# Kernel optimization log

Hardware: AMD Instinct MI355X
Metric: run time of the kernel (lower is better)

## Reference

```python
import jax, jax.numpy as jnp
import numpy as np

# Static hyperparameters (match init_kwargs)
PAD = 4          # one_side_pad_length
KL = 9           # kernel_size (= 2*PAD + 1 so L_out == output_size with stride 1)
STRIDE = 1
NLC = 8          # num_sparse_LC
OUT = 4096       # output_size


def _repeat_lengths():
    padded = OUT + 2 * PAD                      # 4104
    rough = padded // NLC                       # 513
    lens = []
    total = 0
    for i in range(NLC):
        if i == NLC - 1:
            cover = OUT - total
        else:
            cover = rough - 2 * PAD
        lens.append(cover)
        total += cover
    return lens                                  # [505]*7 + [561]


def setup_inputs() -> dict:
    key = jax.random.key(0)
    k1, k2, k3 = jax.random.split(key, 3)
    x = jax.random.normal(k1, (8, 2, 4, 64, 4096), dtype=jnp.float32)
    # weight: (dim_d, dim_k, out, in, num_sparse_LC, 1, kernel_size)
    weight = jax.random.normal(k2, (2, 4, 64, 64, 8, 1, 9), dtype=jnp.float32) * 0.05
    # conv_bias_param: (dim_d, dim_k, out, num_sparse_LC, 1)
    conv_bias_param = jax.random.normal(k3, (2, 4, 64, 8, 1), dtype=jnp.float32) * 0.02
    return {"x": x, "weight": weight, "conv_bias_param": conv_bias_param}


def reference(x, weight, conv_bias_param):
    # x: (b, d, k, in, L)
    x_pad = jnp.pad(x, ((0, 0), (0, 0), (0, 0), (0, 0), (PAD, PAD)))
    # unfold(-1, KL, 1): x_unf[..., l, f] = x_pad[..., l + f]; shape (b,d,k,in,OUT,KL)
    x_unf = jnp.stack([x_pad[..., f:f + OUT] for f in range(KL)], axis=-1)
    lens = _repeat_lengths()
    outs = []
    start = 0
    for i in range(NLC):  # small fixed loop over segments (avoids repeated-weight materialization)
        ln = lens[i]
        w = weight[:, :, :, :, i, 0, :]                 # (d, k, o, in, kl)
        xs = x_unf[:, :, :, :, start:start + ln, :]     # (b, d, k, in, ln, kl)
        o = jnp.einsum('dkoif,bdkilf->bdkol', w, xs)    # (b, d, k, o, ln)
        o = o + conv_bias_param[None, :, :, :, i, :]    # bias broadcasts over b and l
        outs.append(o)
        start += ln
    return jnp.concatenate(outs, axis=-1)               # (b, d, k, o, OUT)
```

## Files before the change

kernel.cpp:

```cpp
#include <hip/hip_runtime.h>

typedef __attribute__((ext_vector_type(8))) short bf16x8;
typedef __attribute__((ext_vector_type(4))) float f32x4;

#define WT2_BYTES (8ull * 8 * 9 * 8192)

static __device__ __forceinline__ ushort f2bf(float f) {
    union { float f; unsigned u; } v; v.f = f;
    unsigned r = v.u + 0x7FFF + ((v.u >> 16) & 1);
    return (ushort)(r >> 16);
}
static __device__ __forceinline__ unsigned cvtpk(float a, float b) {
    unsigned r;
    asm("v_cvt_pk_bf16_f32 %0, %1, %2" : "=v"(r) : "v"(a), "v"(b));
    return r;
}

__global__ __launch_bounds__(256) void wprep3_kernel(const float* __restrict__ w,
                                                     ushort* __restrict__ wt) {
    __shared__ float raw[4608];
    __shared__ ushort row[72 * 64];
    int bid = blockIdx.x;
    int dk = bid >> 6, o = bid & 63;
    const float* src = w + (size_t)bid * 4608;
    int t = threadIdx.x;
    #pragma unroll
    for (int j = 0; j < 18; ++j) raw[t + 256 * j] = src[t + 256 * j];
    __syncthreads();
    int osw = o & 7;
    #pragma unroll
    for (int p = 0; p < 18; ++p) {
        int idx = t + 256 * p;
        int cf = idx >> 6, i = idx & 63;
        int c = cf / 9, f = cf - c * 9;
        row[cf * 64 + ((i >> 3) ^ osw) * 8 + (i & 7)] = f2bf(raw[i * 72 + c * 9 + f]);
    }
    __syncthreads();
    char* wb = (char*)wt + (size_t)dk * 8 * 9 * 8192 + o * 128;
    #pragma unroll
    for (int q = 0; q < 3; ++q) {
        int idx = q * 256 + t;
        if (idx < 576) {
            int cf = idx >> 3, cc = idx & 7;
            *(uint4*)(wb + (size_t)cf * 8192 + cc * 16) = *(const uint4*)&row[cf * 64 + cc * 8];
        }
    }
}

__global__ __launch_bounds__(512, 4) void conv12_kernel(
    const float* __restrict__ x, const ushort* __restrict__ wt,
    const float* __restrict__ bias, float* __restrict__ out)
{
    __shared__ __align__(16) ushort XL[264 * 64];

    int bid = blockIdx.x;
    int b = bid / 136, rem = bid - b * 136;
    int dk = rem / 17, tile = rem - dk * 17;
    int c, lt;
    if (tile < 14) { c = tile >> 1; lt = tile & 1; } else { c = 7; lt = tile - 14; }
    int Sc = 505 * c, lb = lt << 8;
    int V = ((c == 7) ? 561 : 505) - lb; if (V > 256) V = 256;
    int bdk = b * 8 + dk;
    int R0 = Sc + lb;

    int t = threadIdx.x, lane = t & 63, wv = t >> 6;
    int ln16 = lane & 15, g = lane >> 4;
    int wr = wv >> 1, wc = wv & 1;
    int Lw = wr << 6, Ow = wc << 5;

    int lq = t & 63, ig = t >> 6;
    const float* xb = x + (size_t)bdk * 64 * 4096;
    float4 v[8];
    bool edge = (R0 < 4) || (R0 > 3836);
    if (!edge) {
        const float* xp = xb + (size_t)ig * 8 * 4096 + (R0 - 4 + lq * 4);
        #pragma unroll
        for (int j = 0; j < 8; ++j)
            v[j] = *(const float4*)(xp + (size_t)j * 4096);
    } else {
        #pragma unroll
        for (int j = 0; j < 8; ++j) {
            float* pv = (float*)&v[j];
            #pragma unroll
            for (int k = 0; k < 4; ++k) {
                int xr = R0 - 4 + lq * 4 + k;
                bool ok = (xr >= 0) && (xr < 4096);
                int xc = ok ? xr : 0;
                pv[k] = ok ? xb[(size_t)(ig * 8 + j) * 4096 + xc] : 0.0f;
            }
        }
    }
    float hv[8]; int rh = 0, igh = 0;
    if (t < 64) {
        rh = 256 + (t >> 3);
        igh = t & 7;
        int xr = R0 - 4 + rh;
        bool okh = xr < 4096;
        int xc = okh ? xr : 0;
        const float* xh = xb + (size_t)igh * 8 * 4096 + xc;
        #pragma unroll
        for (int j = 0; j < 8; ++j) hv[j] = okh ? xh[(size_t)j * 4096] : 0.0f;
    }

    const char* wsl = (const char*)wt + (size_t)(dk * 8 + c) * 9 * 8192;
    int wo[2][2];
    #pragma unroll
    for (int s = 0; s < 2; ++s)
        #pragma unroll
        for (int nf = 0; nf < 2; ++nf)
            wo[s][nf] = (Ow + nf * 16 + ln16) * 128 + (((s * 4 + g) ^ (ln16 & 7)) * 16);

    bf16x8 w0[2][2], w1[2][2];
    auto loadW = [&](bf16x8 (&d)[2][2], int f) {
        const char* bp = wsl + (size_t)f * 8192;
        #pragma unroll
        for (int s = 0; s < 2; ++s)
            #pragma unroll
            for (int nf = 0; nf < 2; ++nf)
                d[s][nf] = *(const bf16x8*)(bp + wo[s][nf]);
    };
    loadW(w0, 0);

    #pragma unroll
    for (int k = 0; k < 4; ++k) {
        int r = lq * 4 + k;
        uint4 A;
        A.x = cvtpk(((const float*)&v[0])[k], ((const float*)&v[1])[k]);
        A.y = cvtpk(((const float*)&v[2])[k], ((const float*)&v[3])[k]);
        A.z = cvtpk(((const float*)&v[4])[k], ((const float*)&v[5])[k]);
        A.w = cvtpk(((const float*)&v[6])[k], ((const float*)&v[7])[k]);
        *(uint4*)((char*)XL + r * 128 + ((ig ^ (r & 7)) * 16)) = A;
    }
    if (t < 64) {
        uint4 A;
        A.x = cvtpk(hv[0], hv[1]); A.y = cvtpk(hv[2], hv[3]);
        A.z = cvtpk(hv[4], hv[5]); A.w = cvtpk(hv[6], hv[7]);
        *(uint4*)((char*)XL + rh * 128 + ((igh ^ (rh & 7)) * 16)) = A;
    }
    loadW(w1, 1);

    asm volatile("s_waitcnt lgkmcnt(0)" ::: "memory");
    __syncthreads();

    f32x4 acc[4][2];
    #pragma unroll
    for (int a0 = 0; a0 < 4; ++a0)
        #pragma unroll
        for (int a1 = 0; a1 < 2; ++a1) acc[a0][a1] = (f32x4){0.f, 0.f, 0.f, 0.f};

    auto tap = [&](int f, bf16x8 (&wf)[2][2]) {
        int rbase = Lw + ln16 + f;
        int swz = rbase & 7;
        #pragma unroll
        for (int s = 0; s < 2; ++s) {
            int cof = ((s * 4 + g) ^ swz) * 16;
            bf16x8 av[4];
            #pragma unroll
            for (int mf = 0; mf < 4; ++mf)
                av[mf] = *(const bf16x8*)((const char*)XL + (rbase + mf * 16) * 128 + cof);
            __builtin_amdgcn_s_setprio(1);
            #pragma unroll
            for (int mf = 0; mf < 4; ++mf)
                #pragma unroll
                for (int nf = 0; nf < 2; ++nf)
                    acc[mf][nf] = __builtin_amdgcn_mfma_f32_16x16x32_bf16(av[mf], wf[s][nf], acc[mf][nf], 0, 0, 0);
            __builtin_amdgcn_s_setprio(0);
        }
    };

    tap(0, w0); loadW(w0, 2);
    tap(1, w1); loadW(w1, 3);
    tap(2, w0); loadW(w0, 4);
    tap(3, w1); loadW(w1, 5);
    tap(4, w0); loadW(w0, 6);
    tap(5, w1); loadW(w1, 7);
    tap(6, w0); loadW(w0, 8);
    tap(7, w1);
    tap(8, w0);

    float* ob = out + ((size_t)(bdk * 64)) * 4096 + Sc + lb;
    #pragma unroll
    for (int nf = 0; nf < 2; ++nf) {
        int o = Ow + nf * 16 + ln16;
        float bvs = bias[(dk * 64 + o) * 8 + c];
        #pragma unroll
        for (int mf = 0; mf < 4; ++mf) {
            int l = Lw + mf * 16 + g * 4;
            f32x4 vv = acc[mf][nf];
            vv[0] += bvs; vv[1] += bvs; vv[2] += bvs; vv[3] += bvs;
            if (l + 4 <= V) {
                *(f32x4*)(ob + (size_t)o * 4096 + l) = vv;
            } else if (l < V) {
                #pragma unroll
                for (int r = 0; r < 4; ++r)
                    if (l + r < V) ob[(size_t)o * 4096 + l + r] = vv[r];
            }
        }
    }
}

extern "C" void kernel_launch(void* const* d_in, const int* in_sizes, int n_in,
                              void* d_out, int out_size, void* d_ws, size_t ws_size,
                              hipStream_t stream) {
    const float* x    = (const float*)d_in[0];
    const float* wgt  = (const float*)d_in[1];
    const float* bias = (const float*)d_in[2];
    float* out        = (float*)d_out;
    ushort* wt2       = (ushort*)d_ws;

    hipLaunchKernelGGL(wprep3_kernel, dim3(512), dim3(256), 0, stream, wgt, wt2);
    hipLaunchKernelGGL(conv12_kernel, dim3(1088), dim3(512), 0, stream, x, wt2, bias, out);
}
```

Baseline: 49.34 us.

## Process two tiles per block with double-buffered LDS to overlap loads

```diff
diff --git a/kernel.cpp b/kernel.cpp
--- a/kernel.cpp
+++ b/kernel.cpp
@@ -47,62 +47,29 @@
     }
 }
 
-__global__ __launch_bounds__(512, 4) void conv12_kernel(
+__global__ __launch_bounds__(512, 4) void conv13_kernel(
     const float* __restrict__ x, const ushort* __restrict__ wt,
     const float* __restrict__ bias, float* __restrict__ out)
 {
-    __shared__ __align__(16) ushort XL[264 * 64];
-
-    int bid = blockIdx.x;
-    int b = bid / 136, rem = bid - b * 136;
-    int dk = rem / 17, tile = rem - dk * 17;
-    int c, lt;
-    if (tile < 14) { c = tile >> 1; lt = tile & 1; } else { c = 7; lt = tile - 14; }
-    int Sc = 505 * c, lb = lt << 8;
-    int V = ((c == 7) ? 561 : 505) - lb; if (V > 256) V = 256;
-    int bdk = b * 8 + dk;
-    int R0 = Sc + lb;
+    __shared__ __align__(16) ushort XL[2][264 * 64];
 
     int t = threadIdx.x, lane = t & 63, wv = t >> 6;
     int ln16 = lane & 15, g = lane >> 4;
     int wr = wv >> 1, wc = wv & 1;
     int Lw = wr << 6, Ow = wc << 5;
-
     int lq = t & 63, ig = t >> 6;
-    const float* xb = x + (size_t)bdk * 64 * 4096;
-    float4 v[8];
-    bool edge = (R0 < 4) || (R0 > 3836);
-    if (!edge) {
-        const float* xp = xb + (size_t)ig * 8 * 4096 + (R0 - 4 + lq * 4);
-        #pragma unroll
-        for (int j = 0; j < 8; ++j)
-            v[j] = *(const float4*)(xp + (size_t)j * 4096);
-    } else {
-        #pragma unroll
-        for (int j = 0; j < 8; ++j) {
-            float* pv = (float*)&v[j];
-            #pragma unroll
-            for (int k = 0; k < 4; ++k) {
-                int xr = R0 - 4 + lq * 4 + k;
-                bool ok = (xr >= 0) && (xr < 4096);
-                int xc = ok ? xr : 0;
-                pv[k] = ok ? xb[(size_t)(ig * 8 + j) * 4096 + xc] : 0.0f;
-            }
-        }
-    }
-    float hv[8]; int rh = 0, igh = 0;
-    if (t < 64) {
-        rh = 256 + (t >> 3);
-        igh = t & 7;
-        int xr = R0 - 4 + rh;
-        bool okh = xr < 4096;
-        int xc = okh ? xr : 0;
-        const float* xh = xb + (size_t)igh * 8 * 4096 + xc;
-        #pragma unroll
-        for (int j = 0; j < 8; ++j) hv[j] = okh ? xh[(size_t)j * 4096] : 0.0f;
-    }
-
-    const char* wsl = (const char*)wt + (size_t)(dk * 8 + c) * 9 * 8192;
+
+    auto dec = [&](int tid, int& bdk, int& dk, int& c, int& V, int& R0) {
+        int b = tid / 136, rem = tid - b * 136;
+        dk = rem / 17; int tile = rem - dk * 17;
+        int lt;
+        if (tile < 14) { c = tile >> 1; lt = tile & 1; } else { c = 7; lt = tile - 14; }
+        int lb = lt << 8;
+        V = ((c == 7) ? 561 : 505) - lb; if (V > 256) V = 256;
+        R0 = 505 * c + lb;
+        bdk = b * 8 + dk;
+    };
+
     int wo[2][2];
     #pragma unroll
     for (int s = 0; s < 2; ++s)
@@ -110,6 +77,7 @@
         for (int nf = 0; nf < 2; ++nf)
             wo[s][nf] = (Ow + nf * 16 + ln16) * 128 + (((s * 4 + g) ^ (ln16 & 7)) * 16);
 
+    const char* wsl = nullptr;
     bf16x8 w0[2][2], w1[2][2];
     auto loadW = [&](bf16x8 (&d)[2][2], int f) {
         const char* bp = wsl + (size_t)f * 8192;
@@ -119,36 +87,63 @@
             for (int nf = 0; nf < 2; ++nf)
                 d[s][nf] = *(const bf16x8*)(bp + wo[s][nf]);
     };
-    loadW(w0, 0);
-
-    #pragma unroll
-    for (int k = 0; k < 4; ++k) {
-        int r = lq * 4 + k;
-        uint4 A;
-        A.x = cvtpk(((const float*)&v[0])[k], ((const float*)&v[1])[k]);
-        A.y = cvtpk(((const float*)&v[2])[k], ((const float*)&v[3])[k]);
-        A.z = cvtpk(((const float*)&v[4])[k], ((const float*)&v[5])[k]);
-        A.w = cvtpk(((const float*)&v[6])[k], ((const float*)&v[7])[k]);
-        *(uint4*)((char*)XL + r * 128 + ((ig ^ (r & 7)) * 16)) = A;
-    }
-    if (t < 64) {
-        uint4 A;
-        A.x = cvtpk(hv[0], hv[1]); A.y = cvtpk(hv[2], hv[3]);
-        A.z = cvtpk(hv[4], hv[5]); A.w = cvtpk(hv[6], hv[7]);
-        *(uint4*)((char*)XL + rh * 128 + ((igh ^ (rh & 7)) * 16)) = A;
-    }
-    loadW(w1, 1);
-
-    asm volatile("s_waitcnt lgkmcnt(0)" ::: "memory");
-    __syncthreads();
+
+    float4 vA[4], vB[4]; float hv[8];
+    auto issueHalf = [&](int bdkX, int R0X, int h, float4 (&v)[4]) {
+        const float* xb = x + (size_t)bdkX * 64 * 4096;
+        bool edge = (R0X < 4) || (R0X > 3836);
+        if (!edge) {
+            const float* xp = xb + (size_t)(ig * 8 + h * 4) * 4096 + (R0X - 4 + lq * 4);
+            #pragma unroll
+            for (int j = 0; j < 4; ++j)
+                v[j] = *(const float4*)(xp + (size_t)j * 4096);
+        } else {
+            #pragma unroll
+            for (int j = 0; j < 4; ++j) {
+                float* pv = (float*)&v[j];
+                #pragma unroll
+                for (int k = 0; k < 4; ++k) {
+                    int xr = R0X - 4 + lq * 4 + k;
+                    bool ok = (xr >= 0) && (xr < 4096);
+                    int xc = ok ? xr : 0;
+                    pv[k] = ok ? xb[(size_t)(ig * 8 + h * 4 + j) * 4096 + xc] : 0.0f;
+                }
+            }
+        }
+    };
+    auto issueHalo = [&](int bdkX, int R0X) {
+        if (t < 64) {
+            int rh = 256 + (t >> 3), igh = t & 7;
+            int xr = R0X - 4 + rh;
+            bool okh = xr < 4096;
+            int xc = okh ? xr : 0;
+            const float* xh = x + (size_t)bdkX * 64 * 4096 + (size_t)igh * 8 * 4096 + xc;
+            #pragma unroll
+            for (int j = 0; j < 8; ++j) hv[j] = okh ? xh[(size_t)j * 4096] : 0.0f;
+        }
+    };
+    auto writeTile = [&](ushort* dst) {
+        #pragma unroll
+        for (int k = 0; k < 4; ++k) {
+            int r = lq * 4 + k;
+            uint4 A;
+            A.x = cvtpk(((const float*)&vA[0])[k], ((const float*)&vA[1])[k]);
+            A.y = cvtpk(((const float*)&vA[2])[k], ((const float*)&vA[3])[k]);
+            A.z = cvtpk(((const float*)&vB[0])[k], ((const float*)&vB[1])[k]);
+            A.w = cvtpk(((const float*)&vB[2])[k], ((const float*)&vB[3])[k]);
+            *(uint4*)((char*)dst + r * 128 + ((ig ^ (r & 7)) * 16)) = A;
+        }
+        if (t < 64) {
+            int rh = 256 + (t >> 3), igh = t & 7;
+            uint4 A;
+            A.x = cvtpk(hv[0], hv[1]); A.y = cvtpk(hv[2], hv[3]);
+            A.z = cvtpk(hv[4], hv[5]); A.w = cvtpk(hv[6], hv[7]);
+            *(uint4*)((char*)dst + rh * 128 + ((igh ^ (rh & 7)) * 16)) = A;
+        }
+    };
 
     f32x4 acc[4][2];
-    #pragma unroll
-    for (int a0 = 0; a0 < 4; ++a0)
-        #pragma unroll
-        for (int a1 = 0; a1 < 2; ++a1) acc[a0][a1] = (f32x4){0.f, 0.f, 0.f, 0.f};
-
-    auto tap = [&](int f, bf16x8 (&wf)[2][2]) {
+    auto tap = [&](const char* xbuf, int f, bf16x8 (&wf)[2][2]) {
         int rbase = Lw + ln16 + f;
         int swz = rbase & 7;
         #pragma unroll
@@ -157,7 +152,7 @@
             bf16x8 av[4];
             #pragma unroll
             for (int mf = 0; mf < 4; ++mf)
-                av[mf] = *(const bf16x8*)((const char*)XL + (rbase + mf * 16) * 128 + cof);
+                av[mf] = *(const bf16x8*)(xbuf + (rbase + mf * 16) * 128 + cof);
             __builtin_amdgcn_s_setprio(1);
             #pragma unroll
             for (int mf = 0; mf < 4; ++mf)
@@ -167,36 +162,82 @@
             __builtin_amdgcn_s_setprio(0);
         }
     };
-
-    tap(0, w0); loadW(w0, 2);
-    tap(1, w1); loadW(w1, 3);
-    tap(2, w0); loadW(w0, 4);
-    tap(3, w1); loadW(w1, 5);
-    tap(4, w0); loadW(w0, 6);
-    tap(5, w1); loadW(w1, 7);
-    tap(6, w0); loadW(w0, 8);
-    tap(7, w1);
-    tap(8, w0);
-
-    float* ob = out + ((size_t)(bdk * 64)) * 4096 + Sc + lb;
-    #pragma unroll
-    for (int nf = 0; nf < 2; ++nf) {
-        int o = Ow + nf * 16 + ln16;
-        float bvs = bias[(dk * 64 + o) * 8 + c];
-        #pragma unroll
-        for (int mf = 0; mf < 4; ++mf) {
-            int l = Lw + mf * 16 + g * 4;
-            f32x4 vv = acc[mf][nf];
-            vv[0] += bvs; vv[1] += bvs; vv[2] += bvs; vv[3] += bvs;
-            if (l + 4 <= V) {
-                *(f32x4*)(ob + (size_t)o * 4096 + l) = vv;
-            } else if (l < V) {
-                #pragma unroll
-                for (int r = 0; r < 4; ++r)
-                    if (l + r < V) ob[(size_t)o * 4096 + l + r] = vv[r];
+    auto epilogue = [&](int bdk, int dk, int c, int V, int R0) {
+        float* ob = out + ((size_t)(bdk * 64)) * 4096 + R0;
+        #pragma unroll
+        for (int nf = 0; nf < 2; ++nf) {
+            int o = Ow + nf * 16 + ln16;
+            float bvs = bias[(dk * 64 + o) * 8 + c];
+            #pragma unroll
+            for (int mf = 0; mf < 4; ++mf) {
+                int l = Lw + mf * 16 + g * 4;
+                f32x4 vv = acc[mf][nf];
+                vv[0] += bvs; vv[1] += bvs; vv[2] += bvs; vv[3] += bvs;
+                if (l + 4 <= V) {
+                    *(f32x4*)(ob + (size_t)o * 4096 + l) = vv;
+                } else if (l < V) {
+                    #pragma unroll
+                    for (int r = 0; r < 4; ++r)
+                        if (l + r < V) ob[(size_t)o * 4096 + l + r] = vv[r];
+                }
             }
         }
-    }
+    };
+
+    int t0 = 2 * blockIdx.x, t1 = t0 + 1;
+    int bdk0, dk0, c0, V0, R00, bdk1, dk1, c1, V1, R01;
+    dec(t0, bdk0, dk0, c0, V0, R00);
+    dec(t1, bdk1, dk1, c1, V1, R01);
+
+    issueHalf(bdk0, R00, 0, vA);
+    issueHalf(bdk0, R00, 1, vB);
+    issueHalo(bdk0, R00);
+    writeTile(XL[0]);
+    __syncthreads();
+
+    wsl = (const char*)wt + (size_t)(dk0 * 8 + c0) * 9 * 8192;
+    loadW(w0, 0); loadW(w1, 1);
+    #pragma unroll
+    for (int a0 = 0; a0 < 4; ++a0)
+        #pragma unroll
+        for (int a1 = 0; a1 < 2; ++a1) acc[a0][a1] = (f32x4){0.f, 0.f, 0.f, 0.f};
+
+    issueHalf(bdk1, R01, 0, vA);
+    __builtin_amdgcn_sched_barrier(0);
+    const char* xc = (const char*)XL[0];
+    tap(xc, 0, w0); loadW(w0, 2);
+    tap(xc, 1, w1); loadW(w1, 3);
+    tap(xc, 2, w0); loadW(w0, 4);
+    tap(xc, 3, w1); loadW(w1, 5);
+    issueHalf(bdk1, R01, 1, vB);
+    issueHalo(bdk1, R01);
+    __builtin_amdgcn_sched_barrier(0);
+    tap(xc, 4, w0); loadW(w0, 6);
+    tap(xc, 5, w1); loadW(w1, 7);
+    tap(xc, 6, w0); loadW(w0, 8);
+    tap(xc, 7, w1);
+    tap(xc, 8, w0);
+    epilogue(bdk0, dk0, c0, V0, R00);
+    writeTile(XL[1]);
+    __syncthreads();
+
+    wsl = (const char*)wt + (size_t)(dk1 * 8 + c1) * 9 * 8192;
+    loadW(w0, 0); loadW(w1, 1);
+    #pragma unroll
+    for (int a0 = 0; a0 < 4; ++a0)
+        #pragma unroll
+        for (int a1 = 0; a1 < 2; ++a1) acc[a0][a1] = (f32x4){0.f, 0.f, 0.f, 0.f};
+    xc = (const char*)XL[1];
+    tap(xc, 0, w0); loadW(w0, 2);
+    tap(xc, 1, w1); loadW(w1, 3);
+    tap(xc, 2, w0); loadW(w0, 4);
+    tap(xc, 3, w1); loadW(w1, 5);
+    tap(xc, 4, w0); loadW(w0, 6);
+    tap(xc, 5, w1); loadW(w1, 7);
+    tap(xc, 6, w0); loadW(w0, 8);
+    tap(xc, 7, w1);
+    tap(xc, 8, w0);
+    epilogue(bdk1, dk1, c1, V1, R01);
 }
 
 extern "C" void kernel_launch(void* const* d_in, const int* in_sizes, int n_in,
@@ -209,5 +250,5 @@
     ushort* wt2       = (ushort*)d_ws;
 
     hipLaunchKernelGGL(wprep3_kernel, dim3(512), dim3(256), 0, stream, wgt, wt2);
-    hipLaunchKernelGGL(conv12_kernel, dim3(1088), dim3(512), 0, stream, x, wt2, bias, out);
-}
+    hipLaunchKernelGGL(conv13_kernel, dim3(544), dim3(512), 0, stream, x, wt2, bias, out);
+}
```

Measured after the change: 75.43 us. 52.9% more time.

## Pre-transpose x to padded bf16 in prep kernel; drop LDS staging in conv

Applied to the files above, without the earlier changes.

```diff
diff --git a/kernel.cpp b/kernel.cpp
--- a/kernel.cpp
+++ b/kernel.cpp
@@ -3,6 +3,8 @@
 typedef __attribute__((ext_vector_type(8))) short bf16x8;
 typedef __attribute__((ext_vector_type(4))) float f32x4;
 
+#define XT_ROWS 4104
+#define XT_STRIDE ((size_t)XT_ROWS * 128)
 #define WT2_BYTES (8ull * 8 * 9 * 8192)
 
 static __device__ __forceinline__ ushort f2bf(float f) {
@@ -16,43 +18,86 @@
     return r;
 }
 
-__global__ __launch_bounds__(256) void wprep3_kernel(const float* __restrict__ w,
-                                                     ushort* __restrict__ wt) {
+__global__ __launch_bounds__(256) void prep_kernel(const float* __restrict__ w,
+                                                   const float* __restrict__ x,
+                                                   ushort* __restrict__ wt,
+                                                   ushort* __restrict__ xT) {
     __shared__ float raw[4608];
     __shared__ ushort row[72 * 64];
+    __shared__ ushort XB[128 * 72];
     int bid = blockIdx.x;
-    int dk = bid >> 6, o = bid & 63;
-    const float* src = w + (size_t)bid * 4608;
     int t = threadIdx.x;
-    #pragma unroll
-    for (int j = 0; j < 18; ++j) raw[t + 256 * j] = src[t + 256 * j];
-    __syncthreads();
-    int osw = o & 7;
-    #pragma unroll
-    for (int p = 0; p < 18; ++p) {
-        int idx = t + 256 * p;
-        int cf = idx >> 6, i = idx & 63;
-        int c = cf / 9, f = cf - c * 9;
-        row[cf * 64 + ((i >> 3) ^ osw) * 8 + (i & 7)] = f2bf(raw[i * 72 + c * 9 + f]);
+    if (bid < 512) {
+        int dk = bid >> 6, o = bid & 63;
+        const float* src = w + (size_t)bid * 4608;
+        #pragma unroll
+        for (int j = 0; j < 18; ++j) raw[t + 256 * j] = src[t + 256 * j];
+        __syncthreads();
+        int osw = o & 7;
+        #pragma unroll
+        for (int p = 0; p < 18; ++p) {
+            int idx = t + 256 * p;
+            int cf = idx >> 6, i = idx & 63;
+            int c = cf / 9, f = cf - c * 9;
+            row[cf * 64 + ((i >> 3) ^ osw) * 8 + (i & 7)] = f2bf(raw[i * 72 + c * 9 + f]);
+        }
+        __syncthreads();
+        char* wb = (char*)wt + (size_t)dk * 8 * 9 * 8192 + o * 128;
+        #pragma unroll
+        for (int q = 0; q < 3; ++q) {
+            int idx = q * 256 + t;
+            if (idx < 576) {
+                int cf = idx >> 3, cc = idx & 7;
+                *(uint4*)(wb + (size_t)cf * 8192 + cc * 16) = *(const uint4*)&row[cf * 64 + cc * 8];
+            }
+        }
+    } else {
+        int bid2 = bid - 512;
+        int bdk = bid2 >> 5;
+        int lt  = bid2 & 31;
+        int lq = t & 31, ig = t >> 5;
+        int L0 = lt * 128;
+        const float* xb = x + (size_t)bdk * 64 * 4096 + L0 + lq * 4;
+        float4 v[8];
+        #pragma unroll
+        for (int j = 0; j < 8; ++j)
+            v[j] = *(const float4*)(xb + (size_t)(ig * 8 + j) * 4096);
+        #pragma unroll
+        for (int k = 0; k < 4; ++k) {
+            uint4 pk;
+            pk.x = cvtpk(((const float*)&v[0])[k], ((const float*)&v[1])[k]);
+            pk.y = cvtpk(((const float*)&v[2])[k], ((const float*)&v[3])[k]);
+            pk.z = cvtpk(((const float*)&v[4])[k], ((const float*)&v[5])[k]);
+            pk.w = cvtpk(((const float*)&v[6])[k], ((const float*)&v[7])[k]);
+            *(uint4*)&XB[(lq * 4 + k) * 72 + ig * 8] = pk;
+        }
+        __syncthreads();
+        char* xrb = (char*)xT + (size_t)bdk * XT_STRIDE;
+        #pragma unroll
+        for (int it = 0; it < 4; ++it) {
+            int idx = it * 256 + t;
+            int r = idx >> 3, cc = idx & 7;
+            uint4 vv = *(const uint4*)&XB[r * 72 + cc * 8];
+            int rowB = L0 + r + 4;
+            *(uint4*)(xrb + (size_t)rowB * 128 + ((cc ^ (rowB & 7)) * 16)) = vv;
+        }
+        if (lt == 0 && t < 32) {
+            int r = t >> 3, cc = t & 7;
+            uint4 z; z.x = z.y = z.z = z.w = 0u;
+            *(uint4*)(xrb + (size_t)r * 128 + ((cc ^ (r & 7)) * 16)) = z;
+        }
+        if (lt == 31 && t < 32) {
+            int r = 4100 + (t >> 3), cc = t & 7;
+            uint4 z; z.x = z.y = z.z = z.w = 0u;
+            *(uint4*)(xrb + (size_t)r * 128 + ((cc ^ (r & 7)) * 16)) = z;
+        }
     }
-    __syncthreads();
-    char* wb = (char*)wt + (size_t)dk * 8 * 9 * 8192 + o * 128;
-    #pragma unroll
-    for (int q = 0; q < 3; ++q) {
-        int idx = q * 256 + t;
-        if (idx < 576) {
-            int cf = idx >> 3, cc = idx & 7;
-            *(uint4*)(wb + (size_t)cf * 8192 + cc * 16) = *(const uint4*)&row[cf * 64 + cc * 8];
-        }
-    }
-}
-
-__global__ __launch_bounds__(512, 4) void conv12_kernel(
-    const float* __restrict__ x, const ushort* __restrict__ wt,
+}
+
+__global__ __launch_bounds__(512, 4) void conv15_kernel(
+    const ushort* __restrict__ xT, const ushort* __restrict__ wt,
     const float* __restrict__ bias, float* __restrict__ out)
 {
-    __shared__ __align__(16) ushort XL[264 * 64];
-
     int bid = blockIdx.x;
     int b = bid / 136, rem = bid - b * 136;
     int dk = rem / 17, tile = rem - dk * 17;
@@ -68,41 +113,10 @@
     int wr = wv >> 1, wc = wv & 1;
     int Lw = wr << 6, Ow = wc << 5;
 
-    int lq = t & 63, ig = t >> 6;
-    const float* xb = x + (size_t)bdk * 64 * 4096;
-    float4 v[8];
-    bool edge = (R0 < 4) || (R0 > 3836);
-    if (!edge) {
-        const float* xp = xb + (size_t)ig * 8 * 4096 + (R0 - 4 + lq * 4);
-        #pragma unroll
-        for (int j = 0; j < 8; ++j)
-            v[j] = *(const float4*)(xp + (size_t)j * 4096);
-    } else {
-        #pragma unroll
-        for (int j = 0; j < 8; ++j) {
-            float* pv = (float*)&v[j];
-            #pragma unroll
-            for (int k = 0; k < 4; ++k) {
-                int xr = R0 - 4 + lq * 4 + k;
-                bool ok = (xr >= 0) && (xr < 4096);
-                int xc = ok ? xr : 0;
-                pv[k] = ok ? xb[(size_t)(ig * 8 + j) * 4096 + xc] : 0.0f;
-            }
-        }
-    }
-    float hv[8]; int rh = 0, igh = 0;
-    if (t < 64) {
-        rh = 256 + (t >> 3);
-        igh = t & 7;
-        int xr = R0 - 4 + rh;
-        bool okh = xr < 4096;
-        int xc = okh ? xr : 0;
-        const float* xh = xb + (size_t)igh * 8 * 4096 + xc;
-        #pragma unroll
-        for (int j = 0; j < 8; ++j) hv[j] = okh ? xh[(size_t)j * 4096] : 0.0f;
-    }
-
+    const char* xtb = (const char*)xT + (size_t)bdk * XT_STRIDE;
     const char* wsl = (const char*)wt + (size_t)(dk * 8 + c) * 9 * 8192;
+    int qbase = R0 + Lw + ln16;
+
     int wo[2][2];
     #pragma unroll
     for (int s = 0; s < 2; ++s)
@@ -110,7 +124,18 @@
         for (int nf = 0; nf < 2; ++nf)
             wo[s][nf] = (Ow + nf * 16 + ln16) * 128 + (((s * 4 + g) ^ (ln16 & 7)) * 16);
 
-    bf16x8 w0[2][2], w1[2][2];
+    bf16x8 A0[2][4], A1[2][4], w0[2][2], w1[2][2];
+    auto loadA = [&](bf16x8 (&d)[2][4], int f) {
+        const char* rp = xtb + (size_t)(qbase + f) * 128;
+        int k7 = (qbase + f) & 7;
+        #pragma unroll
+        for (int s = 0; s < 2; ++s) {
+            int cof = ((s * 4 + g) ^ k7) * 16;
+            #pragma unroll
+            for (int mf = 0; mf < 4; ++mf)
+                d[s][mf] = *(const bf16x8*)(rp + mf * 2048 + cof);
+        }
+    };
     auto loadW = [&](bf16x8 (&d)[2][2], int f) {
         const char* bp = wsl + (size_t)f * 8192;
         #pragma unroll
@@ -119,28 +144,6 @@
             for (int nf = 0; nf < 2; ++nf)
                 d[s][nf] = *(const bf16x8*)(bp + wo[s][nf]);
     };
-    loadW(w0, 0);
-
-    #pragma unroll
-    for (int k = 0; k < 4; ++k) {
-        int r = lq * 4 + k;
-        uint4 A;
-        A.x = cvtpk(((const float*)&v[0])[k], ((const float*)&v[1])[k]);
-        A.y = cvtpk(((const float*)&v[2])[k], ((const float*)&v[3])[k]);
-        A.z = cvtpk(((const float*)&v[4])[k], ((const float*)&v[5])[k]);
-        A.w = cvtpk(((const float*)&v[6])[k], ((const float*)&v[7])[k]);
-        *(uint4*)((char*)XL + r * 128 + ((ig ^ (r & 7)) * 16)) = A;
-    }
-    if (t < 64) {
-        uint4 A;
-        A.x = cvtpk(hv[0], hv[1]); A.y = cvtpk(hv[2], hv[3]);
-        A.z = cvtpk(hv[4], hv[5]); A.w = cvtpk(hv[6], hv[7]);
-        *(uint4*)((char*)XL + rh * 128 + ((igh ^ (rh & 7)) * 16)) = A;
-    }
-    loadW(w1, 1);
-
-    asm volatile("s_waitcnt lgkmcnt(0)" ::: "memory");
-    __syncthreads();
 
     f32x4 acc[4][2];
     #pragma unroll
@@ -148,35 +151,28 @@
         #pragma unroll
         for (int a1 = 0; a1 < 2; ++a1) acc[a0][a1] = (f32x4){0.f, 0.f, 0.f, 0.f};
 
-    auto tap = [&](int f, bf16x8 (&wf)[2][2]) {
-        int rbase = Lw + ln16 + f;
-        int swz = rbase & 7;
-        #pragma unroll
-        for (int s = 0; s < 2; ++s) {
-            int cof = ((s * 4 + g) ^ swz) * 16;
-            bf16x8 av[4];
-            #pragma unroll
-            for (int mf = 0; mf < 4; ++mf)
-                av[mf] = *(const bf16x8*)((const char*)XL + (rbase + mf * 16) * 128 + cof);
-            __builtin_amdgcn_s_setprio(1);
+    auto tap = [&](bf16x8 (&A)[2][4], bf16x8 (&wf)[2][2]) {
+        #pragma unroll
+        for (int s = 0; s < 2; ++s)
             #pragma unroll
             for (int mf = 0; mf < 4; ++mf)
                 #pragma unroll
                 for (int nf = 0; nf < 2; ++nf)
-                    acc[mf][nf] = __builtin_amdgcn_mfma_f32_16x16x32_bf16(av[mf], wf[s][nf], acc[mf][nf], 0, 0, 0);
-            __builtin_amdgcn_s_setprio(0);
-        }
+                    acc[mf][nf] = __builtin_amdgcn_mfma_f32_16x16x32_bf16(A[s][mf], wf[s][nf], acc[mf][nf], 0, 0, 0);
     };
 
-    tap(0, w0); loadW(w0, 2);
-    tap(1, w1); loadW(w1, 3);
-    tap(2, w0); loadW(w0, 4);
-    tap(3, w1); loadW(w1, 5);
-    tap(4, w0); loadW(w0, 6);
-    tap(5, w1); loadW(w1, 7);
-    tap(6, w0); loadW(w0, 8);
-    tap(7, w1);
-    tap(8, w0);
+    loadA(A0, 0); loadW(w0, 0);
+    loadA(A1, 1); loadW(w1, 1);
+
+    tap(A0, w0); loadA(A0, 2); loadW(w0, 2);
+    tap(A1, w1); loadA(A1, 3); loadW(w1, 3);
+    tap(A0, w0); loadA(A0, 4); loadW(w0, 4);
+    tap(A1, w1); loadA(A1, 5); loadW(w1, 5);
+    tap(A0, w0); loadA(A0, 6); loadW(w0, 6);
+    tap(A1, w1); loadA(A1, 7); loadW(w1, 7);
+    tap(A0, w0); loadA(A0, 8); loadW(w0, 8);
+    tap(A1, w1);
+    tap(A0, w0);
 
     float* ob = out + ((size_t)(bdk * 64)) * 4096 + Sc + lb;
     #pragma unroll
@@ -207,7 +203,8 @@
     const float* bias = (const float*)d_in[2];
     float* out        = (float*)d_out;
     ushort* wt2       = (ushort*)d_ws;
-
-    hipLaunchKernelGGL(wprep3_kernel, dim3(512), dim3(256), 0, stream, wgt, wt2);
-    hipLaunchKernelGGL(conv12_kernel, dim3(1088), dim3(512), 0, stream, x, wt2, bias, out);
-}
+    ushort* xT        = (ushort*)((char*)d_ws + WT2_BYTES);
+
+    hipLaunchKernelGGL(prep_kernel, dim3(2560), dim3(256), 0, stream, wgt, x, wt2, xT);
+    hipLaunchKernelGGL(conv15_kernel, dim3(1088), dim3(512), 0, stream, xT, wt2, bias, out);
+}
```

Result: slower. 93.46 us (+89.4%).

## Use persistent warp-specialized blocks with double-buffered LDS staging of input tiles

Applied to the files above, without the earlier changes.

```diff
diff --git a/kernel.cpp b/kernel.cpp
--- a/kernel.cpp
+++ b/kernel.cpp
@@ -47,154 +47,192 @@
     }
 }
 
-__global__ __launch_bounds__(512, 4) void conv12_kernel(
+__global__ __launch_bounds__(320, 4) void conv18_kernel(
     const float* __restrict__ x, const ushort* __restrict__ wt,
     const float* __restrict__ bias, float* __restrict__ out)
 {
-    __shared__ __align__(16) ushort XL[264 * 64];
-
-    int bid = blockIdx.x;
-    int b = bid / 136, rem = bid - b * 136;
-    int dk = rem / 17, tile = rem - dk * 17;
-    int c, lt;
-    if (tile < 14) { c = tile >> 1; lt = tile & 1; } else { c = 7; lt = tile - 14; }
-    int Sc = 505 * c, lb = lt << 8;
-    int V = ((c == 7) ? 561 : 505) - lb; if (V > 256) V = 256;
-    int bdk = b * 8 + dk;
-    int R0 = Sc + lb;
-
+    __shared__ __align__(16) ushort XL[2][136 * 64];
+    __shared__ int flg[4];
+
+    const int GS = 704;
     int t = threadIdx.x, lane = t & 63, wv = t >> 6;
     int ln16 = lane & 15, g = lane >> 4;
-    int wr = wv >> 1, wc = wv & 1;
-    int Lw = wr << 6, Ow = wc << 5;
-
-    int lq = t & 63, ig = t >> 6;
-    const float* xb = x + (size_t)bdk * 64 * 4096;
-    float4 v[8];
-    bool edge = (R0 < 4) || (R0 > 3836);
-    if (!edge) {
-        const float* xp = xb + (size_t)ig * 8 * 4096 + (R0 - 4 + lq * 4);
+
+    auto dec = [&](int tid, int& bdk, int& dk, int& c, int& V, int& R0) {
+        bdk = tid / 33; int tile = tid - bdk * 33;
+        dk = bdk & 7;
+        int lt;
+        if (tile < 28) { c = tile >> 2; lt = tile & 3; } else { c = 7; lt = tile - 28; }
+        int lb = lt << 7;
+        V = ((c == 7) ? 561 : 505) - lb; if (V > 128) V = 128;
+        R0 = 505 * c + lb;
+    };
+
+    auto stage_part = [&](int tt, int bdkX, int R0X, ushort* dst) {
+        int lq = tt & 31, ig = tt >> 5;
+        const float* xb = x + (size_t)bdkX * 64 * 4096;
+        float4 v[8];
+        bool edge = (R0X < 4) || (R0X > 3964);
+        if (!edge) {
+            const float* xp = xb + (size_t)ig * 8 * 4096 + (R0X - 4 + lq * 4);
+            #pragma unroll
+            for (int j = 0; j < 8; ++j) v[j] = *(const float4*)(xp + (size_t)j * 4096);
+        } else {
+            #pragma unroll
+            for (int j = 0; j < 8; ++j) {
+                float* pv = (float*)&v[j];
+                #pragma unroll
+                for (int k = 0; k < 4; ++k) {
+                    int xr = R0X - 4 + lq * 4 + k;
+                    bool ok = (xr >= 0) && (xr < 4096);
+                    int xc = ok ? xr : 0;
+                    pv[k] = ok ? xb[(size_t)(ig * 8 + j) * 4096 + xc] : 0.0f;
+                }
+            }
+        }
         #pragma unroll
-        for (int j = 0; j < 8; ++j)
-            v[j] = *(const float4*)(xp + (size_t)j * 4096);
-    } else {
-        #pragma unroll
-        for (int j = 0; j < 8; ++j) {
-            float* pv = (float*)&v[j];
-            #pragma unroll
-            for (int k = 0; k < 4; ++k) {
-                int xr = R0 - 4 + lq * 4 + k;
-                bool ok = (xr >= 0) && (xr < 4096);
-                int xc = ok ? xr : 0;
-                pv[k] = ok ? xb[(size_t)(ig * 8 + j) * 4096 + xc] : 0.0f;
-            }
-        }
-    }
-    float hv[8]; int rh = 0, igh = 0;
-    if (t < 64) {
-        rh = 256 + (t >> 3);
-        igh = t & 7;
-        int xr = R0 - 4 + rh;
+        for (int k = 0; k < 4; ++k) {
+            int r = lq * 4 + k;
+            uint4 A;
+            A.x = cvtpk(((const float*)&v[0])[k], ((const float*)&v[1])[k]);
+            A.y = cvtpk(((const float*)&v[2])[k], ((const float*)&v[3])[k]);
+            A.z = cvtpk(((const float*)&v[4])[k], ((const float*)&v[5])[k]);
+            A.w = cvtpk(((const float*)&v[6])[k], ((const float*)&v[7])[k]);
+            *(uint4*)((char*)dst + r * 128 + ((ig ^ (r & 7)) * 16)) = A;
+        }
+    };
+    auto stage_halo = [&](int tt, int bdkX, int R0X, ushort* dst) {
+        int rh = 128 + (tt >> 3), igh = tt & 7;
+        int xr = R0X - 4 + rh;
         bool okh = xr < 4096;
         int xc = okh ? xr : 0;
-        const float* xh = xb + (size_t)igh * 8 * 4096 + xc;
+        const float* xh = x + (size_t)bdkX * 64 * 4096 + (size_t)igh * 8 * 4096 + xc;
+        float hv[8];
         #pragma unroll
         for (int j = 0; j < 8; ++j) hv[j] = okh ? xh[(size_t)j * 4096] : 0.0f;
-    }
-
-    const char* wsl = (const char*)wt + (size_t)(dk * 8 + c) * 9 * 8192;
-    int wo[2][2];
-    #pragma unroll
-    for (int s = 0; s < 2; ++s)
-        #pragma unroll
-        for (int nf = 0; nf < 2; ++nf)
-            wo[s][nf] = (Ow + nf * 16 + ln16) * 128 + (((s * 4 + g) ^ (ln16 & 7)) * 16);
-
-    bf16x8 w0[2][2], w1[2][2];
-    auto loadW = [&](bf16x8 (&d)[2][2], int f) {
-        const char* bp = wsl + (size_t)f * 8192;
-        #pragma unroll
-        for (int s = 0; s < 2; ++s)
-            #pragma unroll
-            for (int nf = 0; nf < 2; ++nf)
-                d[s][nf] = *(const bf16x8*)(bp + wo[s][nf]);
-    };
-    loadW(w0, 0);
-
-    #pragma unroll
-    for (int k = 0; k < 4; ++k) {
-        int r = lq * 4 + k;
-        uint4 A;
-        A.x = cvtpk(((const float*)&v[0])[k], ((const float*)&v[1])[k]);
-        A.y = cvtpk(((const float*)&v[2])[k], ((const float*)&v[3])[k]);
-        A.z = cvtpk(((const float*)&v[4])[k], ((const float*)&v[5])[k]);
-        A.w = cvtpk(((const float*)&v[6])[k], ((const float*)&v[7])[k]);
-        *(uint4*)((char*)XL + r * 128 + ((ig ^ (r & 7)) * 16)) = A;
-    }
-    if (t < 64) {
         uint4 A;
         A.x = cvtpk(hv[0], hv[1]); A.y = cvtpk(hv[2], hv[3]);
         A.z = cvtpk(hv[4], hv[5]); A.w = cvtpk(hv[6], hv[7]);
-        *(uint4*)((char*)XL + rh * 128 + ((igh ^ (rh & 7)) * 16)) = A;
-    }
-    loadW(w1, 1);
-
-    asm volatile("s_waitcnt lgkmcnt(0)" ::: "memory");
+        *(uint4*)((char*)dst + rh * 128 + ((igh ^ (rh & 7)) * 16)) = A;
+    };
+
+    int tid0 = blockIdx.x;
+    int bdk0, dk0, c0, V0, R00;
+    dec(tid0, bdk0, dk0, c0, V0, R00);
+
+    if (t < 4) flg[t] = 0;
+    if (t < 256) stage_part(t, bdk0, R00, XL[0]);
+    if (t < 64)  stage_halo(t, bdk0, R00, XL[0]);
     __syncthreads();
 
-    f32x4 acc[4][2];
-    #pragma unroll
-    for (int a0 = 0; a0 < 4; ++a0)
+    if (wv < 4) {
+        int wr = wv >> 1, wc = wv & 1;
+        int Lw = wr << 6, Ow = wc << 5;
+        int wo[2][2];
         #pragma unroll
-        for (int a1 = 0; a1 < 2; ++a1) acc[a0][a1] = (f32x4){0.f, 0.f, 0.f, 0.f};
-
-    auto tap = [&](int f, bf16x8 (&wf)[2][2]) {
-        int rbase = Lw + ln16 + f;
-        int swz = rbase & 7;
-        #pragma unroll
-        for (int s = 0; s < 2; ++s) {
-            int cof = ((s * 4 + g) ^ swz) * 16;
-            bf16x8 av[4];
-            #pragma unroll
-            for (int mf = 0; mf < 4; ++mf)
-                av[mf] = *(const bf16x8*)((const char*)XL + (rbase + mf * 16) * 128 + cof);
-            __builtin_amdgcn_s_setprio(1);
-            #pragma unroll
-            for (int mf = 0; mf < 4; ++mf)
-                #pragma unroll
-                for (int nf = 0; nf < 2; ++nf)
-                    acc[mf][nf] = __builtin_amdgcn_mfma_f32_16x16x32_bf16(av[mf], wf[s][nf], acc[mf][nf], 0, 0, 0);
-            __builtin_amdgcn_s_setprio(0);
-        }
-    };
-
-    tap(0, w0); loadW(w0, 2);
-    tap(1, w1); loadW(w1, 3);
-    tap(2, w0); loadW(w0, 4);
-    tap(3, w1); loadW(w1, 5);
-    tap(4, w0); loadW(w0, 6);
-    tap(5, w1); loadW(w1, 7);
-    tap(6, w0); loadW(w0, 8);
-    tap(7, w1);
-    tap(8, w0);
-
-    float* ob = out + ((size_t)(bdk * 64)) * 4096 + Sc + lb;
-    #pragma unroll
-    for (int nf = 0; nf < 2; ++nf) {
-        int o = Ow + nf * 16 + ln16;
-        float bvs = bias[(dk * 64 + o) * 8 + c];
-        #pragma unroll
-        for (int mf = 0; mf < 4; ++mf) {
-            int l = Lw + mf * 16 + g * 4;
-            f32x4 vv = acc[mf][nf];
-            vv[0] += bvs; vv[1] += bvs; vv[2] += bvs; vv[3] += bvs;
-            if (l + 4 <= V) {
-                *(f32x4*)(ob + (size_t)o * 4096 + l) = vv;
-            } else if (l < V) {
-                #pragma unroll
-                for (int r = 0; r < 4; ++r)
-                    if (l + r < V) ob[(size_t)o * 4096 + l + r] = vv[r];
+        for (int s = 0; s < 2; ++s)
+            #pragma unroll
+            for (int nf = 0; nf < 2; ++nf)
+                wo[s][nf] = (Ow + nf * 16 + ln16) * 128 + (((s * 4 + g) ^ (ln16 & 7)) * 16);
+
+        int tid = tid0, bdk = bdk0, dk = dk0, c = c0, V = V0, R0 = R00;
+        #pragma unroll 1
+        for (int k = 0; k < 3; ++k) {
+            int p = k & 1;
+            if (k > 0) {
+                int tgt = (k + 1) >> 1;
+                while (__hip_atomic_load(&flg[p], __ATOMIC_ACQUIRE, __HIP_MEMORY_SCOPE_WORKGROUP) < tgt)
+                    __builtin_amdgcn_s_sleep(8);
             }
+            const char* wsl = (const char*)wt + (size_t)(dk * 8 + c) * 9 * 8192;
+            const char* xc_ = (const char*)XL[p];
+
+            bf16x8 w0[2][2], w1[2][2];
+            auto loadW = [&](bf16x8 (&d)[2][2], int f) {
+                const char* bp = wsl + (size_t)f * 8192;
+                #pragma unroll
+                for (int s = 0; s < 2; ++s)
+                    #pragma unroll
+                    for (int nf = 0; nf < 2; ++nf)
+                        d[s][nf] = *(const bf16x8*)(bp + wo[s][nf]);
+            };
+            f32x4 acc[4][2];
+            #pragma unroll
+            for (int a0 = 0; a0 < 4; ++a0)
+                #pragma unroll
+                for (int a1 = 0; a1 < 2; ++a1) acc[a0][a1] = (f32x4){0.f, 0.f, 0.f, 0.f};
+
+            auto tap = [&](int f, bf16x8 (&wf)[2][2]) {
+                int rbase = Lw + ln16 + f;
+                int swz = rbase & 7;
+                #pragma unroll
+                for (int s = 0; s < 2; ++s) {
+                    int cof = ((s * 4 + g) ^ swz) * 16;
+                    bf16x8 av[4];
+                    #pragma unroll
+                    for (int mf = 0; mf < 4; ++mf)
+                        av[mf] = *(const bf16x8*)(xc_ + (rbase + mf * 16) * 128 + cof);
+                    __builtin_amdgcn_s_setprio(1);
+                    #pragma unroll
+                    for (int mf = 0; mf < 4; ++mf)
+                        #pragma unroll
+                        for (int nf = 0; nf < 2; ++nf)
+                            acc[mf][nf] = __builtin_amdgcn_mfma_f32_16x16x32_bf16(av[mf], wf[s][nf], acc[mf][nf], 0, 0, 0);
+                    __builtin_amdgcn_s_setprio(0);
+                }
+            };
+            loadW(w0, 0); loadW(w1, 1);
+            tap(0, w0); loadW(w0, 2);
+            tap(1, w1); loadW(w1, 3);
+            tap(2, w0); loadW(w0, 4);
+            tap(3, w1); loadW(w1, 5);
+            tap(4, w0); loadW(w0, 6);
+            tap(5, w1); loadW(w1, 7);
+            tap(6, w0); loadW(w0, 8);
+            tap(7, w1);
+            tap(8, w0);
+
+            asm volatile("s_waitcnt lgkmcnt(0)" ::: "memory");
+            if (lane == 0)
+                __hip_atomic_fetch_add(&flg[2 + p], 1, __ATOMIC_RELEASE, __HIP_MEMORY_SCOPE_WORKGROUP);
+
+            float* ob = out + ((size_t)(bdk * 64)) * 4096 + R0;
+            #pragma unroll
+            for (int nf = 0; nf < 2; ++nf) {
+                int o = Ow + nf * 16 + ln16;
+                float bvs = bias[(dk * 64 + o) * 8 + c];
+                #pragma unroll
+                for (int mf = 0; mf < 4; ++mf) {
+                    int l = Lw + mf * 16 + g * 4;
+                    f32x4 vv = acc[mf][nf];
+                    vv[0] += bvs; vv[1] += bvs; vv[2] += bvs; vv[3] += bvs;
+                    if (l + 4 <= V) {
+                        *(f32x4*)(ob + (size_t)o * 4096 + l) = vv;
+                    } else if (l < V) {
+                        #pragma unroll
+                        for (int r = 0; r < 4; ++r)
+                            if (l + r < V) ob[(size_t)o * 4096 + l + r] = vv[r];
+                    }
+                }
+            }
+            if (k < 2) { tid += GS; dec(tid, bdk, dk, c, V, R0); }
+        }
+    } else {
+        #pragma unroll 1
+        for (int j = 1; j < 3; ++j) {
+            int p = j & 1;
+            int tgt = 4 * (j >> 1);
+            while (__hip_atomic_load(&flg[2 + p], __ATOMIC_ACQUIRE, __HIP_MEMORY_SCOPE_WORKGROUP) < tgt)
+                __builtin_amdgcn_s_sleep(8);
+            int bdkJ, dkJ, cJ, VJ, R0J;
+            dec(tid0 + j * GS, bdkJ, dkJ, cJ, VJ, R0J);
+            #pragma unroll 1
+            for (int h = 0; h < 4; ++h)
+                stage_part(lane + 64 * h, bdkJ, R0J, XL[p]);
+            stage_halo(lane, bdkJ, R0J, XL[p]);
+            asm volatile("s_waitcnt lgkmcnt(0)" ::: "memory");
+            if (lane == 0)
+                __hip_atomic_fetch_add(&flg[p], 1, __ATOMIC_RELEASE, __HIP_MEMORY_SCOPE_WORKGROUP);
         }
     }
 }
@@ -209,5 +247,5 @@
     ushort* wt2       = (ushort*)d_ws;
 
     hipLaunchKernelGGL(wprep3_kernel, dim3(512), dim3(256), 0, stream, wgt, wt2);
-    hipLaunchKernelGGL(conv12_kernel, dim3(1088), dim3(512), 0, stream, x, wt2, bias, out);
-}
+    hipLaunchKernelGGL(conv18_kernel, dim3(704), dim3(320), 0, stream, x, wt2, bias, out);
+}
```

New measurement: 59.07 us. +19.7%, slower.
